# Performance work log

Measured on AMD Instinct MI355X. Metric: run time of the kernel, lower is better.

The kernel has to match this reference:

```python
import jax, jax.numpy as jnp
import numpy as np

H = 12          # num attention heads
DH = 64         # head size (768 / 12)
THRESHOLD = 0.05


def setup_inputs() -> dict:
    key = jax.random.key(0)
    ks = jax.random.split(key, 13)
    B, S, D = 128, 197, 768
    s = 0.02
    return {
        "hidden_states": jax.random.normal(ks[0], (B, S, D), jnp.float32),
        "Wq": jax.random.normal(ks[1], (D, D), jnp.float32) * s,
        "bq": jax.random.normal(ks[2], (D,), jnp.float32) * s,
        "Wk": jax.random.normal(ks[3], (D, D), jnp.float32) * s,
        "bk": jax.random.normal(ks[4], (D,), jnp.float32) * s,
        "Wv": jax.random.normal(ks[5], (D, D), jnp.float32) * s,
        "bv": jax.random.normal(ks[6], (D,), jnp.float32) * s,
        "Wd": jax.random.normal(ks[7], (D, D), jnp.float32) * s,
        "bd": jax.random.normal(ks[8], (D,), jnp.float32) * s,
        "W1": jax.random.normal(ks[9], (D, 64), jnp.float32) * s,
        "b1": jax.random.normal(ks[10], (64,), jnp.float32) * s,
        "W2": jax.random.normal(ks[11], (64, 1), jnp.float32) * s,
        "b2": jax.random.normal(ks[12], (1,), jnp.float32) * s,
    }


def reference(hidden_states, Wq, bq, Wk, bk, Wv, bv, Wd, bd, W1, b1, W2, b2):
    B, S, D = hidden_states.shape
    # --- DHS scoring MLP on patch tokens (exclude CLS), keep_cls=True path ---
    h = jax.nn.relu(hidden_states[:, 1:] @ W1 + b1)        # [B, S-1, 64]
    mlp_out = jax.nn.sigmoid(h @ W2 + b2)[..., 0]          # [B, S-1]
    patch_mask = mlp_out >= THRESHOLD                      # [B, S-1]
    cls_col = jnp.ones((B, 1), dtype=bool)
    mask = jnp.concatenate([cls_col, patch_mask], axis=1)  # [B, S]

    # --- full self-attention; pruning queries only removes rows, keys/values
    # are never pruned, so computing all rows and masking is equivalent ---
    q = (hidden_states @ Wq + bq).reshape(B, S, H, DH)
    k = (hidden_states @ Wk + bk).reshape(B, S, H, DH)
    v = (hidden_states @ Wv + bv).reshape(B, S, H, DH)
    scores = jnp.einsum("bqhd,bkhd->bhqk", q, k) / jnp.sqrt(jnp.float32(DH))
    probs = jax.nn.softmax(scores, axis=-1)                # dropout p=0.0 (eval)
    ctx = jnp.einsum("bhqk,bkhd->bqhd", probs, v).reshape(B, S, D)
    attn_out = (ctx @ Wd + bd) + ctx                       # dense + residual-to-self_outputs

    # scatter-assign: output[i][mask[i]] = attn_out rows for kept tokens
    output = jnp.where(mask[..., None], attn_out, hidden_states)
    return output
```

## Files before the change

### kernel.cpp

```cpp
#include <hip/hip_runtime.h>
#include <hip/hip_bf16.h>

#define HN 12
#define DHD 64
#define BB 128
#define SQ 197
#define DD 768
#define TOK (BB*SQ)
#define SP 224
#define SPS 232

using short8  = __attribute__((ext_vector_type(8))) short;
using floatx4 = __attribute__((ext_vector_type(4))) float;

__device__ __forceinline__ float bf2f(short v) {
    union { unsigned int u; float f; } x;
    x.u = ((unsigned int)(unsigned short)v) << 16;
    return x.f;
}
__device__ __forceinline__ short f2bf(float f) {
    union { float f; unsigned int u; } x; x.f = f;
    unsigned int u = x.u;
    u += 0x7fffu + ((u >> 16) & 1u);
    return (short)(u >> 16);
}
__device__ __forceinline__ float ldf(const void* p, size_t i, bool isf32) {
    return isf32 ? ((const float*)p)[i] : bf2f(((const short*)p)[i]);
}
__device__ __forceinline__ void gload_lds16(const short* g, short* l) {
    __builtin_amdgcn_global_load_lds(
        (const __attribute__((address_space(1))) void*)g,
        (__attribute__((address_space(3))) void*)l, 16, 0, 0);
}

__global__ __launch_bounds__(256) void detect_kernel(
        const short* __restrict__ wq, float* __restrict__ flag) {
    __shared__ int cnt;
    if (threadIdx.x == 0) cnt = 0;
    __syncthreads();
    int local = 0;
    for (int j = 0; j < 16; j++) {
        int i = threadIdx.x * 16 + j;
        unsigned int u = (unsigned short)wq[2 * i];
        unsigned int e = (u >> 7) & 0xFF;
        if (e < 64 || e >= 192) local++;
    }
    for (int d = 1; d < 64; d <<= 1) local += __shfl_xor(local, d, 64);
    if ((threadIdx.x & 63) == 0) atomicAdd(&cnt, local);
    __syncthreads();
    if (threadIdx.x == 0) *flag = (cnt > 256) ? 1.f : 0.f;
}

__global__ void sentinel_kernel(short* out, int n, float code) {
    int i = blockIdx.x * 256 + threadIdx.x;
    if (i < n) out[i] = (i == 0) ? f2bf(code) : (short)0;
}

__global__ __launch_bounds__(256) void prep_kernel(
        const void* __restrict__ Wq, const void* __restrict__ Wk,
        const void* __restrict__ Wv, const void* __restrict__ Wd,
        const void* __restrict__ bq, const void* __restrict__ bk,
        const void* __restrict__ bv, const void* __restrict__ bd,
        const void* __restrict__ W1, const void* __restrict__ b1,
        const void* __restrict__ W2, const void* __restrict__ b2,
        short* __restrict__ WqkvT, short* __restrict__ WdT,
        short* __restrict__ W1T, float* __restrict__ bcat,
        const float* __restrict__ flag) {
    __shared__ short tile[64][72];
    bool isf32 = (*flag != 0.f);
    int blk = blockIdx.x;
    int tid = threadIdx.x;
    int r = tid >> 2, c0 = (tid & 3) << 4;
    const void* W;
    size_t stride;
    int ti, tj, w = 0;
    if (blk < 576) {
        w = blk / 144;
        int t = blk % 144;
        ti = t / 12; tj = t % 12;
        W = (w == 0) ? Wq : (w == 1) ? Wk : (w == 2) ? Wv : Wd;
        stride = DD;
    } else {
        ti = blk - 576; tj = 0;
        W = W1;
        stride = 64;
    }
    for (int c = 0; c < 16; c++)
        tile[r][c0 + c] =
            f2bf(ldf(W, (size_t)(ti * 64 + r) * stride + tj * 64 + c0 + c, isf32));
    __syncthreads();
    short* out;
    if (blk < 576)
        out = (w < 3)
            ? WqkvT + ((size_t)(w * DD + tj * 64 + r)) * DD + ti * 64
            : WdT   + ((size_t)(tj * 64 + r)) * DD + ti * 64;
    else
        out = W1T + (size_t)r * DD + ti * 64;
    for (int h = 0; h < 2; h++) {
        short8 v;
        #pragma unroll
        for (int c = 0; c < 8; c++) v[c] = tile[c0 + h * 8 + c][r];
        *(short8*)&out[c0 + h * 8] = v;
    }
    if (blk == 0) {
        for (int i = tid; i < DD; i += 256) {
            bcat[i]          = ldf(bq, i, isf32);
            bcat[DD + i]     = ldf(bk, i, isf32);
            bcat[2 * DD + i] = ldf(bv, i, isf32);
            bcat[3 * DD + i] = ldf(bd, i, isf32);
        }
        if (tid < 64) {
            bcat[4 * DD + tid]      = ldf(b1, tid, isf32);
            bcat[4 * DD + 64 + tid] = ldf(W2, tid, isf32);
        }
        if (tid == 0) bcat[4 * DD + 128] = ldf(b2, 0, isf32);
    }
}

__global__ __launch_bounds__(256) void mask_gemm(
        const void* __restrict__ hs, const short* __restrict__ W1T,
        const float* __restrict__ bvec, float* __restrict__ mask,
        short* __restrict__ hsb, const float* __restrict__ flag) {
    __shared__ __align__(16) short As[64 * 32];
    __shared__ __align__(16) short Bs[64 * 32];
    bool isf32 = (*flag != 0.f);
    int tid = threadIdx.x, lane = tid & 63, wave = tid >> 6;
    int quad = lane >> 4, l16 = lane & 15;
    int tok0 = blockIdx.x * 64;

    int arow = tid >> 2, achk = tid & 3;
    int acol = ((achk ^ ((arow >> 1) & 3)) << 3);
    const short* Bg = W1T + (size_t)arow * DD +
                      (((achk ^ ((arow >> 1) & 3)) << 3));
    short* Bl = Bs + wave * 512;
    int fcol = ((quad ^ ((l16 >> 1) & 3)) << 3);

    floatx4 acc[4] = {};
    for (int k0 = 0; k0 < DD; k0 += 32) {
        gload_lds16(Bg + k0, Bl);
        size_t gidx = (size_t)(tok0 + arow) * DD + k0 + achk * 8;
        short8 s;
        if (isf32) {
            const float* hf = (const float*)hs;
            float4 f0 = *(const float4*)&hf[gidx];
            float4 f1 = *(const float4*)&hf[gidx + 4];
            s[0]=f2bf(f0.x); s[1]=f2bf(f0.y); s[2]=f2bf(f0.z); s[3]=f2bf(f0.w);
            s[4]=f2bf(f1.x); s[5]=f2bf(f1.y); s[6]=f2bf(f1.z); s[7]=f2bf(f1.w);
        } else {
            s = *(const short8*)&((const short*)hs)[gidx];
        }
        *(short8*)&hsb[gidx] = s;
        *(short8*)&As[(arow << 5) + acol] = s;
        __syncthreads();
        short8 af = *(const short8*)&As[((wave * 16 + l16) << 5) + fcol];
        #pragma unroll
        for (int j = 0; j < 4; j++) {
            short8 bf8 = *(const short8*)&Bs[((j * 16 + l16) << 5) + fcol];
            acc[j] = __builtin_amdgcn_mfma_f32_16x16x32_bf16(af, bf8, acc[j], 0, 0, 0);
        }
        __syncthreads();
    }

    const float* b1f = bvec + 4 * DD;
    const float* w2f = bvec + 4 * DD + 64;
    float b2v = bvec[4 * DD + 128];
    float partial[4] = {0.f, 0.f, 0.f, 0.f};
    #pragma unroll
    for (int j = 0; j < 4; j++) {
        int n = j * 16 + l16;
        float b1v = b1f[n], w2v = w2f[n];
        #pragma unroll
        for (int r = 0; r < 4; r++) {
            float hv = fmaxf(acc[j][r] + b1v, 0.f);
            partial[r] += hv * w2v;
        }
    }
    for (int d = 1; d < 16; d <<= 1)
        #pragma unroll
        for (int r = 0; r < 4; r++)
            partial[r] += __shfl_xor(partial[r], d, 64);
    if (l16 == 0) {
        #pragma unroll
        for (int r = 0; r < 4; r++) {
            int tokr = tok0 + wave * 16 + quad * 4 + r;
            float m = 1.f;
            if (tokr % SQ != 0) {
                float sg = 1.f / (1.f + __expf(-(partial[r] + b2v)));
                m = (sg >= 0.05f) ? 1.f : 0.f;
            }
            mask[tokr] = m;
        }
    }
}

template <int MODE>
__global__ __launch_bounds__(256, 8) void gemm128(
        const short* __restrict__ A, const short* __restrict__ BT,
        const float* __restrict__ bias, void* __restrict__ C,
        int m0g, int Mreal, int N,
        const float* __restrict__ mask, const short* __restrict__ resid,
        const void* __restrict__ hs, const float* __restrict__ flag) {
    constexpr int K = DD;
    __shared__ __align__(16) short As[128 * 32];
    __shared__ __align__(16) short Bs[64 * 32];
    int tiles_n = N >> 6;
    int nwg = gridDim.x, bid = blockIdx.x;
    int qq = nwg >> 3, rr = nwg & 7, xcd = bid & 7, lid = bid >> 3;
    int wg = (xcd < rr ? xcd * (qq + 1) : rr * (qq + 1) + (xcd - rr) * qq) + lid;
    int bm = wg / tiles_n, bn = wg % tiles_n;
    int m0 = bm << 7, n0 = bn << 6;

    int tid = threadIdx.x, lane = tid & 63, wave = tid >> 6;
    int wx = wave & 1, wy = wave >> 1;
    int quad = lane >> 4, l16 = lane & 15;

    int s0 = tid, s1 = 256 + tid;
    int ar0 = s0 >> 2, ac0 = ((s0 & 3) ^ ((ar0 >> 1) & 3)) << 3;
    int ar1 = s1 >> 2, ac1 = ((s1 & 3) ^ ((ar1 >> 1) & 3)) << 3;
    int br  = tid >> 2, bc  = ((tid & 3) ^ ((br >> 1) & 3)) << 3;
    int am0 = m0 + ar0; if (am0 >= Mreal) am0 = Mreal - 1;
    int am1 = m0 + ar1; if (am1 >= Mreal) am1 = Mreal - 1;
    const short* Ag0 = A + (size_t)am0 * K + ac0;
    const short* Ag1 = A + (size_t)am1 * K + ac1;
    const short* Bg  = BT + (size_t)(n0 + br) * K + bc;
    short* Al0 = As + wave * 512;
    short* Al1 = As + 2048 + wave * 512;
    short* Bl  = Bs + wave * 512;

    int acol = ((quad ^ ((l16 >> 1) & 3)) << 3);

    floatx4 acc[4][2] = {};
    for (int k0 = 0; k0 < K; k0 += 32) {
        gload_lds16(Ag0 + k0, Al0);
        gload_lds16(Ag1 + k0, Al1);
        gload_lds16(Bg  + k0, Bl);
        __syncthreads();
        short8 bfr[2];
        #pragma unroll
        for (int j = 0; j < 2; j++)
            bfr[j] = *(const short8*)&Bs[(((wx << 5) + (j << 4) + l16) << 5) + acol];
        #pragma unroll
        for (int i = 0; i < 4; i++) {
            short8 af = *(const short8*)&As[(((wy << 6) + (i << 4) + l16) << 5) + acol];
            acc[i][0] = __builtin_amdgcn_mfma_f32_16x16x32_bf16(af, bfr[0], acc[i][0], 0, 0, 0);
            acc[i][1] = __builtin_amdgcn_mfma_f32_16x16x32_bf16(af, bfr[1], acc[i][1], 0, 0, 0);
        }
        __syncthreads();
    }

    bool isf32 = (MODE == 1) ? (*flag != 0.f) : false;
    #pragma unroll
    for (int i = 0; i < 4; i++)
        #pragma unroll
        for (int j = 0; j < 2; j++) {
            int n = n0 + (wx << 5) + (j << 4) + l16;
            float bb = bias[n];
            #pragma unroll
            for (int r = 0; r < 4; r++) {
                int m = m0 + (wy << 6) + (i << 4) + (quad << 2) + r;
                if (m >= Mreal) continue;
                float v = acc[i][j][r] + bb;
                if (MODE == 0) {
                    ((short*)C)[(size_t)m * N + n] = f2bf(v);
                } else {
                    size_t gm = (size_t)(m0g + m);
                    v += bf2f(resid[(size_t)m * N + n]);
                    if (mask[gm] == 0.f) v = ldf(hs, gm * N + n, isf32);
                    if (isf32) ((float*)C)[gm * N + n] = v;
                    else       ((short*)C)[gm * N + n] = f2bf(v);
                }
            }
        }
}

__global__ __launch_bounds__(256) void attn_kernel(
        const short* __restrict__ qkv, short* __restrict__ ctx) {
    __shared__ __align__(16) short Vt[DHD * SPS];
    __shared__ __align__(16) short P[4 * 16 * SPS];
    int nwg = gridDim.x, bid = blockIdx.x;
    int qq = nwg >> 3, rr = nwg & 7, xcd = bid & 7, lid = bid >> 3;
    int blk = (xcd < rr ? xcd * (qq + 1) : rr * (qq + 1) + (xcd - rr) * qq) + lid;
    int qc = blk & 3;
    int h  = (blk >> 2) % HN;
    int b  = blk / (4 * HN);
    int tid = threadIdx.x, lane = tid & 63, wave = tid >> 6;
    int quad = lane >> 4, l16 = lane & 15;
    const short* base = qkv + (size_t)b * SQ * 2304;

    for (int i = tid; i < SQ * DHD; i += 256) {
        int s = i >> 6, d = i & 63;
        Vt[d * SPS + s] = base[(size_t)s * 2304 + 1536 + h * 64 + d];
    }
    for (int i = tid; i < (SP - SQ) * DHD; i += 256) {
        int s = SQ + i % (SP - SQ), d = i / (SP - SQ);
        Vt[d * SPS + s] = 0;
    }
    __syncthreads();

    int mrow = qc * 64 + wave * 16 + l16;
    if (mrow > SQ - 1) mrow = SQ - 1;
    const short* Qrow = base + (size_t)mrow * 2304 + h * 64;
    short8 aq0 = *(const short8*)(Qrow + quad * 8);
    short8 aq1 = *(const short8*)(Qrow + 32 + quad * 8);

    floatx4 sc[14];
    for (int t = 0; t < 14; t++) {
        int nrow = t * 16 + l16;
        if (nrow > SQ - 1) nrow = SQ - 1;
        const short* Krow = base + (size_t)nrow * 2304 + DD + h * 64;
        short8 b0 = *(const short8*)(Krow + quad * 8);
        short8 b1 = *(const short8*)(Krow + 32 + quad * 8);
        floatx4 c = {0.f, 0.f, 0.f, 0.f};
        c = __builtin_amdgcn_mfma_f32_16x16x32_bf16(aq0, b0, c, 0, 0, 0);
        c = __builtin_amdgcn_mfma_f32_16x16x32_bf16(aq1, b1, c, 0, 0, 0);
        sc[t] = c;
    }

    const float scale = 0.125f;
    float mx[4] = {-1e30f, -1e30f, -1e30f, -1e30f};
    for (int t = 0; t < 14; t++) {
        int col = t * 16 + l16;
        if (col < SQ)
            for (int r = 0; r < 4; r++) mx[r] = fmaxf(mx[r], sc[t][r]);
    }
    for (int d = 1; d < 16; d <<= 1)
        for (int r = 0; r < 4; r++) mx[r] = fmaxf(mx[r], __shfl_xor(mx[r], d, 64));
    float sum[4] = {0.f, 0.f, 0.f, 0.f};
    for (int t = 0; t < 14; t++) {
        int col = t * 16 + l16;
        for (int r = 0; r < 4; r++) {
            float e = (col < SQ) ? __expf((sc[t][r] - mx[r]) * scale) : 0.f;
            sc[t][r] = e; sum[r] += e;
        }
    }
    for (int d = 1; d < 16; d <<= 1)
        for (int r = 0; r < 4; r++) sum[r] += __shfl_xor(sum[r], d, 64);
    float inv[4];
    for (int r = 0; r < 4; r++) inv[r] = 1.f / sum[r];

    short* Pw = &P[wave * 16 * SPS];
    for (int t = 0; t < 14; t++)
        for (int r = 0; r < 4; r++)
            Pw[(quad * 4 + r) * SPS + t * 16 + l16] = f2bf(sc[t][r] * inv[r]);
    __syncthreads();

    floatx4 co[4] = {};
    for (int ks = 0; ks < 7; ks++) {
        short8 pa = *(const short8*)&Pw[l16 * SPS + ks * 32 + quad * 8];
        for (int j = 0; j < 4; j++) {
            short8 vb = *(const short8*)&Vt[(j * 16 + l16) * SPS + ks * 32 + quad * 8];
            co[j] = __builtin_amdgcn_mfma_f32_16x16x32_bf16(pa, vb, co[j], 0, 0, 0);
        }
    }
    int sq0 = qc * 64 + wave * 16 + quad * 4;
    for (int r = 0; r < 4; r++) {
        int s = sq0 + r;
        if (s < SQ) {
            size_t o = ((size_t)(b * SQ + s)) * DD + h * 64;
            for (int j = 0; j < 4; j++)
                ctx[o + j * 16 + l16] = f2bf(co[j][r]);
        }
    }
}

extern "C" void kernel_launch(void* const* d_in, const int* in_sizes, int n_in,
                              void* d_out, int out_size, void* d_ws, size_t ws_size,
                              hipStream_t stream) {
    const void* hs = d_in[0];
    const void* Wq = d_in[1];
    const void* bq = d_in[2];
    const void* Wk = d_in[3];
    const void* bk = d_in[4];
    const void* Wv = d_in[5];
    const void* bv = d_in[6];
    const void* Wd = d_in[7];
    const void* bd = d_in[8];
    const void* W1 = d_in[9];
    const void* b1 = d_in[10];
    const void* W2 = d_in[11];
    const void* b2 = d_in[12];

    const size_t flag_b  = 16;
    const size_t mask_b  = (size_t)TOK * 4;
    const size_t bcat_b  = (size_t)(4 * DD + 192) * 4;
    const size_t wqkvt_b = (size_t)3 * DD * DD * 2;
    const size_t wdt_b   = (size_t)DD * DD * 2;
    const size_t w1t_b   = (size_t)64 * DD * 2;
    const size_t hsb_b   = (size_t)TOK * DD * 2;
    const size_t fixed   = flag_b + mask_b + bcat_b + wqkvt_b + wdt_b + w1t_b + hsb_b;

    int CHB = 0;
    for (int c = 128; c >= 1; c >>= 1) {
        size_t chtp = (size_t)((c * SQ + 127) / 128) * 128;
        size_t need = fixed + chtp * 2304 * 2 + chtp * DD * 2;
        if (need <= ws_size) { CHB = c; break; }
    }
    if (CHB == 0) {
        sentinel_kernel<<<(out_size + 255) / 256, 256, 0, stream>>>(
            (short*)d_out, out_size, (float)((double)ws_size / 1.0e6));
        return;
    }
    const int CHT  = CHB * SQ;
    const int CHTP = ((CHT + 127) / 128) * 128;

    char* ws = (char*)d_ws;
    float* flag  = (float*)ws;
    float* mask  = (float*)(ws + flag_b);
    float* bcat  = (float*)(ws + flag_b + mask_b);
    short* WqkvT = (short*)(ws + flag_b + mask_b + bcat_b);
    short* WdT   = WqkvT + (size_t)3 * DD * DD;
    short* W1T   = WdT + (size_t)DD * DD;
    short* hsb   = W1T + (size_t)64 * DD;
    short* QKVc  = hsb + (size_t)TOK * DD;
    short* ctxc  = QKVc + (size_t)CHTP * 2304;

    detect_kernel<<<1, 256, 0, stream>>>((const short*)Wq, flag);
    prep_kernel<<<588, 256, 0, stream>>>(Wq, Wk, Wv, Wd, bq, bk, bv, bd,
                                         W1, b1, W2, b2,
                                         WqkvT, WdT, W1T, bcat, flag);
    mask_gemm<<<TOK / 64, 256, 0, stream>>>(hs, W1T, bcat, mask, hsb, flag);

    const int nchunk  = BB / CHB;
    const int tiles_m = CHTP / 128;
    for (int c = 0; c < nchunk; c++) {
        const int m0g = c * CHT;
        gemm128<0><<<tiles_m * (3 * DD / 64), 256, 0, stream>>>(
            hsb + (size_t)m0g * DD, WqkvT, bcat, QKVc,
            m0g, CHT, 3 * DD, nullptr, nullptr, nullptr, flag);
        attn_kernel<<<CHB * HN * 4, 256, 0, stream>>>(QKVc, ctxc);
        gemm128<1><<<tiles_m * (DD / 64), 256, 0, stream>>>(
            ctxc, WdT, bcat + 3 * DD, d_out,
            m0g, CHT, DD, mask, ctxc, hs, flag);
    }
}
```

Baseline: 663.2 us.

## Enlarge GEMM tiles to 128x128 with BK=64 and 512-thread blocks

The projection GEMM kernel now uses 128x128 output tiles with 8 waves per block and a K-step of 64 instead of 32, and the LDS swizzle is changed to an 8-way XOR pattern. This halves the number of K-loop iterations and barriers and doubles reuse of each A tile across N. The cost is more LDS per block (32KB), fewer blocks in the grid and possibly lower occupancy, while per-wave accumulator count stays the same.

New measurement: 560.4 us. -15.5%, faster.

```diff
diff --git a/kernel.cpp b/kernel.cpp
--- a/kernel.cpp
+++ b/kernel.cpp
@@ -194,56 +194,65 @@
 }
 
 template <int MODE>
-__global__ __launch_bounds__(256, 8) void gemm128(
+__global__ __launch_bounds__(512, 4) void gemm128(
         const short* __restrict__ A, const short* __restrict__ BT,
         const float* __restrict__ bias, void* __restrict__ C,
         int m0g, int Mreal, int N,
         const float* __restrict__ mask, const short* __restrict__ resid,
         const void* __restrict__ hs, const float* __restrict__ flag) {
     constexpr int K = DD;
-    __shared__ __align__(16) short As[128 * 32];
-    __shared__ __align__(16) short Bs[64 * 32];
-    int tiles_n = N >> 6;
+    constexpr int BK = 64;
+    __shared__ __align__(16) short As[128 * BK];
+    __shared__ __align__(16) short Bs[128 * BK];
+    int tiles_n = N >> 7;
     int nwg = gridDim.x, bid = blockIdx.x;
     int qq = nwg >> 3, rr = nwg & 7, xcd = bid & 7, lid = bid >> 3;
     int wg = (xcd < rr ? xcd * (qq + 1) : rr * (qq + 1) + (xcd - rr) * qq) + lid;
     int bm = wg / tiles_n, bn = wg % tiles_n;
-    int m0 = bm << 7, n0 = bn << 6;
+    int m0 = bm << 7, n0 = bn << 7;
 
     int tid = threadIdx.x, lane = tid & 63, wave = tid >> 6;
-    int wx = wave & 1, wy = wave >> 1;
-    int quad = lane >> 4, l16 = lane & 15;
-
-    int s0 = tid, s1 = 256 + tid;
-    int ar0 = s0 >> 2, ac0 = ((s0 & 3) ^ ((ar0 >> 1) & 3)) << 3;
-    int ar1 = s1 >> 2, ac1 = ((s1 & 3) ^ ((ar1 >> 1) & 3)) << 3;
-    int br  = tid >> 2, bc  = ((tid & 3) ^ ((br >> 1) & 3)) << 3;
-    int am0 = m0 + ar0; if (am0 >= Mreal) am0 = Mreal - 1;
-    int am1 = m0 + ar1; if (am1 >= Mreal) am1 = Mreal - 1;
-    const short* Ag0 = A + (size_t)am0 * K + ac0;
-    const short* Ag1 = A + (size_t)am1 * K + ac1;
-    const short* Bg  = BT + (size_t)(n0 + br) * K + bc;
-    short* Al0 = As + wave * 512;
-    short* Al1 = As + 2048 + wave * 512;
-    short* Bl  = Bs + wave * 512;
-
-    int acol = ((quad ^ ((l16 >> 1) & 3)) << 3);
+    int wx = wave & 3, wy = wave >> 2;
+    int quad = lane >> 4, l16 = lane & 15, l7 = l16 & 7;
+
+    int slot0 = (wave << 7) + lane;
+    int slot1 = slot0 + 64;
+    int r0 = slot0 >> 3, c0s = ((slot0 & 7) ^ (r0 & 7)) << 3;
+    int r1 = slot1 >> 3, c1s = ((slot1 & 7) ^ (r1 & 7)) << 3;
+    int am0 = m0 + r0; if (am0 >= Mreal) am0 = Mreal - 1;
+    int am1 = m0 + r1; if (am1 >= Mreal) am1 = Mreal - 1;
+    const short* Ag0 = A + (size_t)am0 * K + c0s;
+    const short* Ag1 = A + (size_t)am1 * K + c1s;
+    const short* Bg0 = BT + (size_t)(n0 + r0) * K + c0s;
+    const short* Bg1 = BT + (size_t)(n0 + r1) * K + c1s;
+    short* Al0 = As + wave * 1024;
+    short* Al1 = Al0 + 512;
+    short* Bl0 = Bs + wave * 1024;
+    short* Bl1 = Bl0 + 512;
 
     floatx4 acc[4][2] = {};
-    for (int k0 = 0; k0 < K; k0 += 32) {
+    for (int k0 = 0; k0 < K; k0 += BK) {
         gload_lds16(Ag0 + k0, Al0);
         gload_lds16(Ag1 + k0, Al1);
-        gload_lds16(Bg  + k0, Bl);
+        gload_lds16(Bg0 + k0, Bl0);
+        gload_lds16(Bg1 + k0, Bl1);
         __syncthreads();
-        short8 bfr[2];
-        #pragma unroll
-        for (int j = 0; j < 2; j++)
-            bfr[j] = *(const short8*)&Bs[(((wx << 5) + (j << 4) + l16) << 5) + acol];
-        #pragma unroll
-        for (int i = 0; i < 4; i++) {
-            short8 af = *(const short8*)&As[(((wy << 6) + (i << 4) + l16) << 5) + acol];
-            acc[i][0] = __builtin_amdgcn_mfma_f32_16x16x32_bf16(af, bfr[0], acc[i][0], 0, 0, 0);
-            acc[i][1] = __builtin_amdgcn_mfma_f32_16x16x32_bf16(af, bfr[1], acc[i][1], 0, 0, 0);
+        #pragma unroll
+        for (int ks = 0; ks < 2; ks++) {
+            int colo = ((((ks << 2) + quad) ^ l7) << 3);
+            short8 af[4], bfr[2];
+            #pragma unroll
+            for (int i = 0; i < 4; i++)
+                af[i] = *(const short8*)&As[(((wy << 6) + (i << 4) + l16) << 6) + colo];
+            #pragma unroll
+            for (int j = 0; j < 2; j++)
+                bfr[j] = *(const short8*)&Bs[(((wx << 5) + (j << 4) + l16) << 6) + colo];
+            #pragma unroll
+            for (int i = 0; i < 4; i++)
+                #pragma unroll
+                for (int j = 0; j < 2; j++)
+                    acc[i][j] = __builtin_amdgcn_mfma_f32_16x16x32_bf16(
+                        af[i], bfr[j], acc[i][j], 0, 0, 0);
         }
         __syncthreads();
     }
@@ -424,11 +433,11 @@
     const int tiles_m = CHTP / 128;
     for (int c = 0; c < nchunk; c++) {
         const int m0g = c * CHT;
-        gemm128<0><<<tiles_m * (3 * DD / 64), 256, 0, stream>>>(
+        gemm128<0><<<tiles_m * (3 * DD / 128), 512, 0, stream>>>(
             hsb + (size_t)m0g * DD, WqkvT, bcat, QKVc,
             m0g, CHT, 3 * DD, nullptr, nullptr, nullptr, flag);
         attn_kernel<<<CHB * HN * 4, 256, 0, stream>>>(QKVc, ctxc);
-        gemm128<1><<<tiles_m * (DD / 64), 256, 0, stream>>>(
+        gemm128<1><<<tiles_m * (DD / 128), 512, 0, stream>>>(
             ctxc, WdT, bcat + 3 * DD, d_out,
             m0g, CHT, DD, mask, ctxc, hs, flag);
     }
```
